# Kernel tuning notes

Hardware: AMD Instinct MI355X
Metric: run time of the kernel (lower is better)

The kernel has to match this reference:

```python
import jax, jax.numpy as jnp
import numpy as np

B, T, DIM = 256, 2048, 64
THETA, MU, SIGMA = 0.1, 0.0, 1.0


def setup_inputs() -> dict:
    key = jax.random.key(0)
    k1, k2 = jax.random.split(key)
    # strictly increasing positive times, shape [B, T, 1]
    dt = jax.random.uniform(k1, (B, T, 1), minval=1e-3, maxval=1e-2, dtype=jnp.float32)
    ts = jnp.cumsum(dt, axis=1)
    # standard normal reparameterization noise for Normal(0, delta_ts).rsample()
    noise = jax.random.normal(k2, (B, T, DIM), dtype=jnp.float32)
    return {"ts": ts, "noise": noise}


def reference(ts, noise):
    h = DIM // 2  # slice_index
    # t_prev: 0 at step 0, ts[:, :-1] afterwards
    t_prev = jnp.concatenate([jnp.zeros_like(ts[:, :1]), ts[:, :-1]], axis=1)  # [B,T,1]
    # Brownian-increment std: sqrt(t_k - t_{k-1})  (sqrt(t_0) at k=0)
    db = jnp.sqrt(ts - t_prev)  # [B,T,1]
    # OU-increment std: sqrt(exp(2*theta*t_k) - exp(2*theta*t_{k-1}))  (exp(0)=1 at k=0)
    dou = jnp.sqrt(jnp.exp(2.0 * THETA * ts) - jnp.exp(2.0 * THETA * t_prev))  # [B,T,1]
    bt = ts.shape[:-1]
    delta = jnp.concatenate([jnp.broadcast_to(db, bt + (h,)),
                             jnp.broadcast_to(dou, bt + (h,))], axis=-1)  # [B,T,DIM]
    invalid = delta <= 0.0
    delta = jnp.where(invalid, delta + 1e-4, delta)
    # rsample = 0 + delta * eps; zero out invalid entries
    r = jnp.where(invalid, 0.0, delta * noise)
    # per-half scaling
    scale = jnp.concatenate([jnp.full((h,), np.sqrt(SIGMA), dtype=r.dtype),
                             jnp.full((h,), SIGMA / np.sqrt(2.0 * THETA), dtype=r.dtype)])
    r = r * scale
    out = jnp.cumsum(r, axis=-2)  # scan along time
    # OU mean-reversion transform on second half
    e = jnp.exp(-THETA * ts)  # [B,T,1]
    ou = e * out[..., h:] + MU * (1.0 - e)
    # normalize=True branch
    bm = out[..., :h] / (SIGMA * jnp.sqrt(ts) + 1e-8)
    ou = ou / (SIGMA * jnp.sqrt((1.0 - jnp.exp(-2.0 * THETA * ts)) / (2.0 * THETA)) + 1e-8)
    return jnp.concatenate([bm, ou], axis=-1)  # [B,T,DIM]
```

## Files before the change

### kernel.cpp

```cpp
#include <hip/hip_runtime.h>
#include <cstddef>

#define B_   256
#define T_   2048
#define DIM_ 64
#define NC_  16
#define CS_  (T_ / NC_)
#define SG_  16
#define SPS_ (CS_ / SG_)
#define OU_SCALE 2.2360679774997896f

__device__ __forceinline__ float2 delta_pair(const float* __restrict__ tsb, int t) {
    float tk = tsb[t];
    float tp = (t == 0) ? 0.0f : tsb[t - 1];
    float dt = tk - tp;
    float db  = sqrtf(dt);
    float dou = sqrtf(expf(0.2f * tp) * expm1f(0.2f * dt));
    float cb = (db  <= 0.0f) ? 0.0f : db;
    float co = (dou <= 0.0f) ? 0.0f : dou * OU_SCALE;
    return make_float2(cb, co);
}

__global__ __launch_bounds__(256) void partial_kernel(
        const float* __restrict__ ts,
        const float* __restrict__ noise,
        float* __restrict__ out)
{
    __shared__ float2 dlt[CS_];
    __shared__ float4 red[SG_][16];

    const int v   = blockIdx.x;
    const int b   = v >> 4;
    const int c   = v & (NC_ - 1);
    const int tid = threadIdx.x;
    const int sg  = tid >> 4;
    const int qi  = tid & 15;
    const int q   = qi << 2;
    const int t0  = c * CS_;

    const size_t rowbase = (size_t)b * T_ * DIM_;
    const float* np = noise + rowbase + (size_t)(t0 + sg * SPS_) * DIM_ + q;
    float4 r[SPS_];
#pragma unroll
    for (int i = 0; i < SPS_; ++i)
        r[i] = *(const float4*)(np + (size_t)i * DIM_);

    const float* tsb = ts + (size_t)b * T_;
    if (tid < CS_) dlt[tid] = delta_pair(tsb, t0 + tid);
    __syncthreads();

    const bool ou = q >= (DIM_ / 2);
    float4 a = make_float4(0.f, 0.f, 0.f, 0.f);
#pragma unroll
    for (int i = 0; i < SPS_; ++i) {
        float2 d2 = dlt[sg * SPS_ + i];
        float d = ou ? d2.y : d2.x;
        a.x = fmaf(d, r[i].x, a.x);
        a.y = fmaf(d, r[i].y, a.y);
        a.z = fmaf(d, r[i].z, a.z);
        a.w = fmaf(d, r[i].w, a.w);
    }
    red[sg][qi] = a;
    __syncthreads();

    if (tid < 16) {
        float4 s = red[0][tid];
#pragma unroll
        for (int k = 1; k < SG_; ++k) {
            float4 t4 = red[k][tid];
            s.x += t4.x; s.y += t4.y; s.z += t4.z; s.w += t4.w;
        }
        *(float4*)(out + rowbase + (size_t)t0 * DIM_ + (tid << 2)) = s;
    }
}

__global__ __launch_bounds__(64) void prefix_kernel(float* __restrict__ out)
{
    const int b = blockIdx.x;
    const int l = threadIdx.x;
    float* p = out + (size_t)b * T_ * DIM_ + l;
    float acc = 0.0f;
#pragma unroll
    for (int c = 0; c < NC_; ++c) {
        const size_t idx = (size_t)c * CS_ * DIM_;
        float v = p[idx];
        p[idx] = acc;
        acc += v;
    }
}

__global__ __launch_bounds__(256) void scan_kernel(
        const float* __restrict__ ts,
        const float* __restrict__ noise,
        float* __restrict__ out)
{
    __shared__ float4 cof[CS_];
    __shared__ float4 red[SG_][16];

    const int v   = blockIdx.x;
    const int b   = v >> 4;
    const int c   = v & (NC_ - 1);
    const int tid = threadIdx.x;
    const int sg  = tid >> 4;
    const int qi  = tid & 15;
    const int q   = qi << 2;
    const int t0  = c * CS_;

    const size_t rowbase = (size_t)b * T_ * DIM_;
    const float* np = noise + rowbase + (size_t)(t0 + sg * SPS_) * DIM_ + q;
    float4 r[SPS_];
#pragma unroll
    for (int i = 0; i < SPS_; ++i)
        r[i] = *(const float4*)(np + (size_t)i * DIM_);

    float4 base = *(const float4*)(out + rowbase + (size_t)t0 * DIM_ + q);

    const float* tsb = ts + (size_t)b * T_;
    if (tid < CS_) {
        int t = t0 + tid;
        float2 d  = delta_pair(tsb, t);
        float tk  = tsb[t];
        float fb  = 1.0f / (sqrtf(tk) + 1e-8f);
        float em  = expf(-0.1f * tk);
        float fo  = em / (sqrtf(-expm1f(-0.2f * tk) * 5.0f) + 1e-8f);
        cof[tid] = make_float4(d.x, d.y, fb, fo);
    }
    __syncthreads();

    const bool ou = q >= (DIM_ / 2);
    float4 s = make_float4(0.f, 0.f, 0.f, 0.f);
#pragma unroll
    for (int i = 0; i < SPS_; ++i) {
        float4 cc = cof[sg * SPS_ + i];
        float d = ou ? cc.y : cc.x;
        r[i].x *= d; r[i].y *= d; r[i].z *= d; r[i].w *= d;
        s.x += r[i].x; s.y += r[i].y; s.z += r[i].z; s.w += r[i].w;
    }
    red[sg][qi] = s;
    __syncthreads();

    float4 acc = base;
    for (int k = 0; k < sg; ++k) {
        float4 p = red[k][qi];
        acc.x += p.x; acc.y += p.y; acc.z += p.z; acc.w += p.w;
    }

    float* op = out + rowbase + (size_t)(t0 + sg * SPS_) * DIM_ + q;
#pragma unroll
    for (int i = 0; i < SPS_; ++i) {
        float4 cc = cof[sg * SPS_ + i];
        float f = ou ? cc.w : cc.z;
        acc.x += r[i].x; acc.y += r[i].y; acc.z += r[i].z; acc.w += r[i].w;
        float4 o = make_float4(acc.x * f, acc.y * f, acc.z * f, acc.w * f);
        *(float4*)(op + (size_t)i * DIM_) = o;
    }
}

extern "C" void kernel_launch(void* const* d_in, const int* in_sizes, int n_in,
                              void* d_out, int out_size, void* d_ws, size_t ws_size,
                              hipStream_t stream) {
    const float* ts    = (const float*)d_in[0];
    const float* noise = (const float*)d_in[1];
    float* out = (float*)d_out;
    (void)d_ws; (void)ws_size; (void)in_sizes; (void)n_in; (void)out_size;

    partial_kernel<<<B_ * NC_, 256, 0, stream>>>(ts, noise, out);
    prefix_kernel <<<B_,       64,  0, stream>>>(out);
    scan_kernel   <<<B_ * NC_, 256, 0, stream>>>(ts, noise, out);
}
```

Before: 253.6 us.

## Fuse chunk partial sums and prefix into one per-batch kernel, skip last chunk

Merges the partial-sum and prefix kernels into a single 1024-thread block per batch row. Each wave sums one chunk, reduces it with cross-lane shuffles, and writes the exclusive prefix directly to the chunk base, which removes one launch and the global round trip. The last chunk's partial sum is never needed, so its noise read is skipped. The scan kernel's output stores become nontemporal. In exchange, the first pass now runs only 256 large blocks, which may lower occupancy and memory-level parallelism for the noise reads.

```diff
diff --git a/kernel.cpp b/kernel.cpp
--- a/kernel.cpp
+++ b/kernel.cpp
@@ -10,6 +10,8 @@
 #define SPS_ (CS_ / SG_)
 #define OU_SCALE 2.2360679774997896f
 
+typedef float nfloat4 __attribute__((ext_vector_type(4)));
+
 __device__ __forceinline__ float2 delta_pair(const float* __restrict__ tsb, int t) {
     float tk = tsb[t];
     float tp = (t == 0) ? 0.0f : tsb[t - 1];
@@ -21,72 +23,55 @@
     return make_float2(cb, co);
 }
 
-__global__ __launch_bounds__(256) void partial_kernel(
+__global__ __launch_bounds__(1024) void base_kernel(
         const float* __restrict__ ts,
         const float* __restrict__ noise,
         float* __restrict__ out)
 {
-    __shared__ float2 dlt[CS_];
-    __shared__ float4 red[SG_][16];
+    __shared__ float2 dlt[T_];
+    __shared__ float  par[NC_][DIM_];
 
-    const int v   = blockIdx.x;
-    const int b   = v >> 4;
-    const int c   = v & (NC_ - 1);
+    const int b   = blockIdx.x;
     const int tid = threadIdx.x;
-    const int sg  = tid >> 4;
-    const int qi  = tid & 15;
-    const int q   = qi << 2;
-    const int t0  = c * CS_;
+    const int w   = tid >> 6;
+    const int l   = tid & 63;
+
+    const float* tsb = ts + (size_t)b * T_;
+    for (int t = tid; t < T_; t += 1024)
+        dlt[t] = delta_pair(tsb, t);
+    __syncthreads();
 
     const size_t rowbase = (size_t)b * T_ * DIM_;
-    const float* np = noise + rowbase + (size_t)(t0 + sg * SPS_) * DIM_ + q;
-    float4 r[SPS_];
-#pragma unroll
-    for (int i = 0; i < SPS_; ++i)
-        r[i] = *(const float4*)(np + (size_t)i * DIM_);
 
-    const float* tsb = ts + (size_t)b * T_;
-    if (tid < CS_) dlt[tid] = delta_pair(tsb, t0 + tid);
+    if (w != NC_ - 1) {
+        const int  g   = l >> 4;
+        const int  dq  = (l & 15) << 2;
+        const bool ouA = (dq >= DIM_ / 2);
+        const int  tb  = w * CS_;
+        float4 a = make_float4(0.f, 0.f, 0.f, 0.f);
+#pragma unroll 8
+        for (int i = 0; i < CS_ / 4; ++i) {
+            const int t = tb + (i << 2) + g;
+            const float4 v = *(const float4*)(noise + rowbase + (size_t)t * DIM_ + dq);
+            const float2 d2 = dlt[t];
+            const float delta = ouA ? d2.y : d2.x;
+            a.x = fmaf(delta, v.x, a.x);
+            a.y = fmaf(delta, v.y, a.y);
+            a.z = fmaf(delta, v.z, a.z);
+            a.w = fmaf(delta, v.w, a.w);
+        }
+        a.x += __shfl_xor(a.x, 16); a.y += __shfl_xor(a.y, 16);
+        a.z += __shfl_xor(a.z, 16); a.w += __shfl_xor(a.w, 16);
+        a.x += __shfl_xor(a.x, 32); a.y += __shfl_xor(a.y, 32);
+        a.z += __shfl_xor(a.z, 32); a.w += __shfl_xor(a.w, 32);
+        if (l < 16) *(float4*)&par[w][l << 2] = a;
+    }
     __syncthreads();
 
-    const bool ou = q >= (DIM_ / 2);
-    float4 a = make_float4(0.f, 0.f, 0.f, 0.f);
-#pragma unroll
-    for (int i = 0; i < SPS_; ++i) {
-        float2 d2 = dlt[sg * SPS_ + i];
-        float d = ou ? d2.y : d2.x;
-        a.x = fmaf(d, r[i].x, a.x);
-        a.y = fmaf(d, r[i].y, a.y);
-        a.z = fmaf(d, r[i].z, a.z);
-        a.w = fmaf(d, r[i].w, a.w);
-    }
-    red[sg][qi] = a;
-    __syncthreads();
-
-    if (tid < 16) {
-        float4 s = red[0][tid];
-#pragma unroll
-        for (int k = 1; k < SG_; ++k) {
-            float4 t4 = red[k][tid];
-            s.x += t4.x; s.y += t4.y; s.z += t4.z; s.w += t4.w;
-        }
-        *(float4*)(out + rowbase + (size_t)t0 * DIM_ + (tid << 2)) = s;
-    }
-}
-
-__global__ __launch_bounds__(64) void prefix_kernel(float* __restrict__ out)
-{
-    const int b = blockIdx.x;
-    const int l = threadIdx.x;
-    float* p = out + (size_t)b * T_ * DIM_ + l;
+    const int c = w;
     float acc = 0.0f;
-#pragma unroll
-    for (int c = 0; c < NC_; ++c) {
-        const size_t idx = (size_t)c * CS_ * DIM_;
-        float v = p[idx];
-        p[idx] = acc;
-        acc += v;
-    }
+    for (int k = 0; k < c; ++k) acc += par[k][l];
+    out[rowbase + (size_t)c * CS_ * DIM_ + l] = acc;
 }
 
 __global__ __launch_bounds__(256) void scan_kernel(
@@ -151,8 +136,8 @@
         float4 cc = cof[sg * SPS_ + i];
         float f = ou ? cc.w : cc.z;
         acc.x += r[i].x; acc.y += r[i].y; acc.z += r[i].z; acc.w += r[i].w;
-        float4 o = make_float4(acc.x * f, acc.y * f, acc.z * f, acc.w * f);
-        *(float4*)(op + (size_t)i * DIM_) = o;
+        nfloat4 o = { acc.x * f, acc.y * f, acc.z * f, acc.w * f };
+        __builtin_nontemporal_store(o, (nfloat4*)(op + (size_t)i * DIM_));
     }
 }
 
@@ -164,7 +149,6 @@
     float* out = (float*)d_out;
     (void)d_ws; (void)ws_size; (void)in_sizes; (void)n_in; (void)out_size;
 
-    partial_kernel<<<B_ * NC_, 256, 0, stream>>>(ts, noise, out);
-    prefix_kernel <<<B_,       64,  0, stream>>>(out);
-    scan_kernel   <<<B_ * NC_, 256, 0, stream>>>(ts, noise, out);
+    base_kernel<<<B_,       1024, 0, stream>>>(ts, noise, out);
+    scan_kernel<<<B_ * NC_, 256,  0, stream>>>(ts, noise, out);
 }
```

Result: slower. 261.5 us (+3.1%).
